# Kernel optimization log

Hardware: AMD Instinct MI355X
Metric: run time of the kernel (lower is better)

The kernel has to match this reference:

```python
import jax, jax.numpy as jnp
import numpy as np

D = 1024      # model dimension
H = 16        # heads
DK = D // H   # head dim
DFF = 4096    # ffn hidden
B, S = 2, 2048
EPS = 1e-6
NEG_SLOPE = 0.01  # torch LeakyReLU default


def setup_inputs() -> dict:
    key = jax.random.key(0)
    ks = jax.random.split(key, 12)
    sd = 1.0 / np.sqrt(D)
    sf = 1.0 / np.sqrt(DFF)
    return {
        "x": jax.random.normal(ks[0], (B, S, D), dtype=jnp.float32),
        "wq": jax.random.uniform(ks[1], (D, D), jnp.float32, -sd, sd),
        "bq": jnp.zeros((D,), jnp.float32),
        "wk": jax.random.uniform(ks[2], (D, D), jnp.float32, -sd, sd),
        "bk": jnp.zeros((D,), jnp.float32),
        "wv": jax.random.uniform(ks[3], (D, D), jnp.float32, -sd, sd),
        "bv": jnp.zeros((D,), jnp.float32),
        "wo": jax.random.uniform(ks[4], (D, D), jnp.float32, -sd, sd),
        "bo": jnp.zeros((D,), jnp.float32),
        "g1": jnp.ones((D,), jnp.float32),
        "b1": jnp.zeros((D,), jnp.float32),
        "w_ff1": jax.random.uniform(ks[5], (D, DFF), jnp.float32, -sd, sd),
        "b_ff1": jnp.zeros((DFF,), jnp.float32),
        "w_ff2": jax.random.uniform(ks[6], (DFF, D), jnp.float32, -sf, sf),
        "b_ff2": jnp.zeros((D,), jnp.float32),
        "g2": jnp.ones((D,), jnp.float32),
        "b2": jnp.zeros((D,), jnp.float32),
    }


def _layernorm(x, g, b):
    mu = jnp.mean(x, axis=-1, keepdims=True)
    var = jnp.mean(jnp.square(x - mu), axis=-1, keepdims=True)
    return (x - mu) * jax.lax.rsqrt(var + EPS) * g + b


def reference(x, wq, bq, wk, bk, wv, bv, wo, bo, g1, b1,
              w_ff1, b_ff1, w_ff2, b_ff2, g2, b2):
    # Multi-head attention
    q = (x @ wq + bq).reshape(B, S, H, DK).transpose(0, 2, 1, 3)  # [B,H,S,DK]
    k = (x @ wk + bk).reshape(B, S, H, DK).transpose(0, 2, 1, 3)
    v = (x @ wv + bv).reshape(B, S, H, DK).transpose(0, 2, 1, 3)
    scores = jnp.einsum('bhqd,bhkd->bhqk', q, k) / np.sqrt(DK)
    attn = jax.nn.softmax(scores, axis=-1)
    ctx = jnp.einsum('bhqk,bhkd->bhqd', attn, v)
    ctx = ctx.transpose(0, 2, 1, 3).reshape(B, S, D)
    attn_out = ctx @ wo + bo
    # residual + LN1 (dropout = identity in eval)
    h = _layernorm(attn_out + x, g1, b1)
    # FFN with LeakyReLU
    ff = jnp.where(h @ w_ff1 + b_ff1 > 0,
                   h @ w_ff1 + b_ff1,
                   NEG_SLOPE * (h @ w_ff1 + b_ff1))
    ff = ff @ w_ff2 + b_ff2
    return _layernorm(ff + h, g2, b2)
```

## Files before the change

### kernel.cpp

```cpp
#include <hip/hip_runtime.h>
#include <math.h>

#define D_MODEL 1024
#define NHEAD   16
#define DKH     64
#define DFF_    4096
#define BB      2
#define SS      2048
#define MTOT    (BB*SS)
#define EPSLN   1e-6f
#define NEG_SLOPE 0.01f

typedef unsigned short u16;
typedef unsigned int   u32;
typedef __bf16 bf16x8 __attribute__((ext_vector_type(8)));
typedef float  f32x4  __attribute__((ext_vector_type(4)));
typedef u16    u16x4  __attribute__((ext_vector_type(4)));

__device__ __forceinline__ u16 f2bf(float f) {
    u32 u = __float_as_uint(f);
    u = (u + 0x7fffu + ((u >> 16) & 1u)) >> 16;
    return (u16)u;
}

__device__ __forceinline__ void gload_lds16(const u16* g, u16* l) {
    __builtin_amdgcn_global_load_lds(
        (const __attribute__((address_space(1))) u32*)g,
        (__attribute__((address_space(3))) u32*)l,
        16, 0, 0);
}

__global__ __launch_bounds__(256)
void f32_to_bf16(const float* __restrict__ in, u16* __restrict__ out) {
    int i = blockIdx.x * 256 + threadIdx.x;
    float4 v = ((const float4*)in)[i];
    u16x4 o = { f2bf(v.x), f2bf(v.y), f2bf(v.z), f2bf(v.w) };
    ((u16x4*)out)[i] = o;
}

__global__ __launch_bounds__(256)
void transpose_w_bf16(const float* __restrict__ W, u16* __restrict__ WT,
                      int K, int N, int out_stride, int out_row_off, float scale)
{
    __shared__ u16 T[64 * 72];
    const int t  = threadIdx.x;
    const int n0 = blockIdx.x * 64;
    const int k0 = blockIdx.y * 64;
    #pragma unroll
    for (int i = 0; i < 4; ++i) {
        int r = i * 16 + (t >> 4);
        int c = (t & 15) * 4;
        float4 v = *(const float4*)&W[(size_t)(k0 + r) * N + n0 + c];
        T[(c + 0) * 72 + r] = f2bf(v.x * scale);
        T[(c + 1) * 72 + r] = f2bf(v.y * scale);
        T[(c + 2) * 72 + r] = f2bf(v.z * scale);
        T[(c + 3) * 72 + r] = f2bf(v.w * scale);
    }
    __syncthreads();
    #pragma unroll
    for (int i = 0; i < 4; ++i) {
        int nr = i * 16 + (t >> 4);
        int kc = (t & 15) * 4;
        u16x4 o = { T[nr*72 + kc], T[nr*72 + kc + 1], T[nr*72 + kc + 2], T[nr*72 + kc + 3] };
        *(u16x4*)&WT[(size_t)(out_row_off + n0 + nr) * out_stride + k0 + kc] = o;
    }
}

__global__ __launch_bounds__(256)
void transpose_v(const u16* __restrict__ QKV, u16* __restrict__ Vt)
{
    __shared__ u16 T[64 * 72];
    const int t  = threadIdx.x;
    const int s0 = blockIdx.x * 64;
    const int bh = blockIdx.y;
    const int b  = bh >> 4, h = bh & 15;
    #pragma unroll
    for (int i = 0; i < 2; ++i) {
        int r = i * 32 + (t >> 3);
        int c = (t & 7) * 8;
        bf16x8 v = *(const bf16x8*)(QKV + ((size_t)b * SS + s0 + r) * 3072 + 2048 + h * 64 + c);
        #pragma unroll
        for (int j = 0; j < 8; ++j) T[(c + j) * 72 + r] = ((const u16*)&v)[j];
    }
    __syncthreads();
    #pragma unroll
    for (int i = 0; i < 2; ++i) {
        int d  = i * 32 + (t >> 3);
        int kc = (t & 7) * 8;
        *(bf16x8*)(Vt + ((size_t)bh * 64 + d) * SS + s0 + kc) = *(const bf16x8*)&T[d * 72 + kc];
    }
}

__global__ __launch_bounds__(256)
void concat_bias(const float* __restrict__ a, const float* __restrict__ b,
                 const float* __restrict__ c, float* __restrict__ out, float qscale) {
    int i = blockIdx.x * 256 + threadIdx.x;
    out[i] = (i < 1024) ? a[i] * qscale : ((i < 2048) ? b[i - 1024] : c[i - 2048]);
}

template<int EPI>
__global__ __launch_bounds__(256)
void gemm_bf16(const u16* __restrict__ A, const u16* __restrict__ BT,
               const float* __restrict__ bias, void* __restrict__ Cout,
               int M, int N, int k_len, int kstride)
{
    __shared__ u16 As[128 * 32];
    __shared__ u16 Bs[128 * 32];
    const int tid  = threadIdx.x;
    const int w    = tid >> 6;
    const int lane = tid & 63;
    const int lm   = lane & 15;
    const int lq   = lane >> 4;
    const int row0 = blockIdx.y * 128;
    const int col0 = blockIdx.x * 128;
    const int k_off = blockIdx.z * k_len;
    const int wrow = (w >> 1) * 64;
    const int wcol = (w & 1) * 64;

    f32x4 acc[4][4] = {};

    const int r_l  = lane >> 2;
    const int q_sw = (lane & 3) ^ ((lane >> 3) & 3);
    const u16* a_src = A  + (size_t)(row0 + w * 32 + r_l) * kstride + k_off + q_sw * 8;
    const u16* b_src = BT + (size_t)(col0 + w * 32 + r_l) * kstride + k_off + q_sw * 8;
    u16* a_dst = &As[(w * 32) * 32];
    u16* b_dst = &Bs[(w * 32) * 32];
    const size_t stepA = (size_t)16 * kstride;

    const int pos = lq ^ ((lm >> 1) & 3);
    const u16* a_rd = &As[(wrow + lm) * 32 + pos * 8];
    const u16* b_rd = &Bs[(wcol + lm) * 32 + pos * 8];

    for (int k0 = 0; k0 < k_len; k0 += 32) {
        gload_lds16(a_src + k0,         a_dst);
        gload_lds16(a_src + k0 + stepA, a_dst + 16 * 32);
        gload_lds16(b_src + k0,         b_dst);
        gload_lds16(b_src + k0 + stepA, b_dst + 16 * 32);
        __syncthreads();
        bf16x8 av[4], bv[4];
        #pragma unroll
        for (int m = 0; m < 4; ++m) av[m] = *(const bf16x8*)(a_rd + m * 16 * 32);
        #pragma unroll
        for (int n = 0; n < 4; ++n) bv[n] = *(const bf16x8*)(b_rd + n * 16 * 32);
        #pragma unroll
        for (int m = 0; m < 4; ++m)
            #pragma unroll
            for (int n = 0; n < 4; ++n)
                acc[m][n] = __builtin_amdgcn_mfma_f32_16x16x32_bf16(av[m], bv[n], acc[m][n], 0, 0, 0);
        __syncthreads();
    }

    float bz[4] = {0.f, 0.f, 0.f, 0.f};
    if (EPI != 3) {
        #pragma unroll
        for (int n = 0; n < 4; ++n) bz[n] = bias[col0 + wcol + n * 16 + lm];
    }
    float* Cz = (float*)Cout + (size_t)blockIdx.z * M * N;

    #pragma unroll
    for (int m = 0; m < 4; ++m) {
        #pragma unroll
        for (int e = 0; e < 4; ++e) {
            int row = row0 + wrow + m * 16 + lq * 4 + e;
            #pragma unroll
            for (int n = 0; n < 4; ++n) {
                int col = col0 + wcol + n * 16 + lm;
                float v = acc[m][n][e] + bz[n];
                if (EPI == 1) v = v > 0.f ? v : NEG_SLOPE * v;
                if (EPI == 3) Cz[(size_t)row * N + col] = v;
                else          ((u16*)Cout)[(size_t)row * N + col] = f2bf(v);
            }
        }
    }
}

__global__ __launch_bounds__(256)
void attn_mfma(const u16* __restrict__ QKV, const u16* __restrict__ Vt,
               u16* __restrict__ ctx)
{
    __shared__ u16 Qs[64 * 72];
    __shared__ u16 Ks[64 * 72];
    __shared__ u16 Vs[64 * 72];
    __shared__ u16 Ps[64 * 72];
    const int tid = threadIdx.x, w = tid >> 6, lane = tid & 63;
    const int lm = lane & 15, lq = lane >> 4;
    const int q0 = blockIdx.x * 64;
    const int bh = blockIdx.y;
    const int b  = bh >> 4, h = bh & 15;
    const size_t row_b = (size_t)b * SS;
    const int ccol = h * DKH;

    const int sr = tid >> 3;
    const int sc = (tid & 7) * 8;

    #pragma unroll
    for (int i = 0; i < 2; ++i) {
        int r = i * 32 + sr;
        *(bf16x8*)&Qs[r * 72 + sc] =
            *(const bf16x8*)(QKV + (row_b + q0 + r) * 3072 + ccol + sc);
    }
    bf16x8 kr[2], vr[2];
    #pragma unroll
    for (int i = 0; i < 2; ++i) {
        int r = i * 32 + sr;
        kr[i] = *(const bf16x8*)(QKV + (row_b + r) * 3072 + 1024 + ccol + sc);
        vr[i] = *(const bf16x8*)(Vt + ((size_t)bh * 64 + r) * SS + sc);
    }
    __syncthreads();
    bf16x8 aq0 = *(const bf16x8*)&Qs[(w * 16 + lm) * 72 + lq * 8];
    bf16x8 aq1 = *(const bf16x8*)&Qs[(w * 16 + lm) * 72 + 32 + lq * 8];

    bf16x8 ones;
    #pragma unroll
    for (int j = 0; j < 8; ++j) ones[j] = (__bf16)1.0f;

    f32x4 o[4] = {};
    f32x4 lacc = {};

    for (int kt = 0; kt < SS / 64; ++kt) {
        __syncthreads();
        #pragma unroll
        for (int i = 0; i < 2; ++i) {
            int r = i * 32 + sr;
            *(bf16x8*)&Ks[r * 72 + sc] = kr[i];
            *(bf16x8*)&Vs[r * 72 + sc] = vr[i];
        }
        const int kn = ((kt + 1) & 31) * 64;
        #pragma unroll
        for (int i = 0; i < 2; ++i) {
            int r = i * 32 + sr;
            kr[i] = *(const bf16x8*)(QKV + (row_b + kn + r) * 3072 + 1024 + ccol + sc);
            vr[i] = *(const bf16x8*)(Vt + ((size_t)bh * 64 + r) * SS + kn + sc);
        }
        __syncthreads();

        f32x4 s[4] = {};
        #pragma unroll
        for (int n = 0; n < 4; ++n) {
            bf16x8 bk0 = *(const bf16x8*)&Ks[(n * 16 + lm) * 72 + lq * 8];
            bf16x8 bk1 = *(const bf16x8*)&Ks[(n * 16 + lm) * 72 + 32 + lq * 8];
            s[n] = __builtin_amdgcn_mfma_f32_16x16x32_bf16(aq0, bk0, s[n], 0, 0, 0);
            s[n] = __builtin_amdgcn_mfma_f32_16x16x32_bf16(aq1, bk1, s[n], 0, 0, 0);
        }
        const int prow = (w * 16 + lq * 4) * 72 + lm;
        #pragma unroll
        for (int n = 0; n < 4; ++n)
            #pragma unroll
            for (int e = 0; e < 4; ++e)
                Ps[prow + e * 72 + n * 16] = f2bf(__builtin_exp2f(s[n][e]));
        __syncthreads();

        bf16x8 ap0 = *(const bf16x8*)&Ps[(w * 16 + lm) * 72 + lq * 8];
        bf16x8 ap1 = *(const bf16x8*)&Ps[(w * 16 + lm) * 72 + 32 + lq * 8];
        #pragma unroll
        for (int n = 0; n < 4; ++n) {
            bf16x8 bv0 = *(const bf16x8*)&Vs[(n * 16 + lm) * 72 + lq * 8];
            bf16x8 bv1 = *(const bf16x8*)&Vs[(n * 16 + lm) * 72 + 32 + lq * 8];
            o[n] = __builtin_amdgcn_mfma_f32_16x16x32_bf16(ap0, bv0, o[n], 0, 0, 0);
            o[n] = __builtin_amdgcn_mfma_f32_16x16x32_bf16(ap1, bv1, o[n], 0, 0, 0);
        }
        lacc = __builtin_amdgcn_mfma_f32_16x16x32_bf16(ap0, ones, lacc, 0, 0, 0);
        lacc = __builtin_amdgcn_mfma_f32_16x16x32_bf16(ap1, ones, lacc, 0, 0, 0);
    }

    #pragma unroll
    for (int e = 0; e < 4; ++e) {
        float inv = 1.0f / lacc[e];
        int row = q0 + w * 16 + lq * 4 + e;
        u16* dst = ctx + (row_b + row) * D_MODEL + ccol;
        #pragma unroll
        for (int n = 0; n < 4; ++n)
            dst[n * 16 + lm] = f2bf(o[n][e] * inv);
    }
}

template<int DUAL>
__global__ __launch_bounds__(256)
void add_ln(const float* __restrict__ C0, const float* __restrict__ C1,
            const float* __restrict__ cbias, const float* __restrict__ resid,
            const float* __restrict__ g, const float* __restrict__ beta,
            float* __restrict__ out, u16* __restrict__ out_bf)
{
    __shared__ float red[8];
    const int row = blockIdx.x;
    const int tid = threadIdx.x;
    float4 v0 = ((const float4*)(C0 + (size_t)row * D_MODEL))[tid];
    float4 v1 = ((const float4*)(C1 + (size_t)row * D_MODEL))[tid];
    float4 cb = ((const float4*)cbias)[tid];
    float4 vr = ((const float4*)(resid + (size_t)row * D_MODEL))[tid];
    float4 v  = { v0.x + v1.x + cb.x + vr.x, v0.y + v1.y + cb.y + vr.y,
                  v0.z + v1.z + cb.z + vr.z, v0.w + v1.w + cb.w + vr.w };
    float s  = v.x + v.y + v.z + v.w;
    float sq = v.x*v.x + v.y*v.y + v.z*v.z + v.w*v.w;
    #pragma unroll
    for (int off = 32; off > 0; off >>= 1) {
        s  += __shfl_down(s,  off, 64);
        sq += __shfl_down(sq, off, 64);
    }
    const int wv = tid >> 6;
    if ((tid & 63) == 0) { red[wv] = s; red[4 + wv] = sq; }
    __syncthreads();
    float st  = red[0] + red[1] + red[2] + red[3];
    float sqt = red[4] + red[5] + red[6] + red[7];
    float mu   = st * (1.0f / D_MODEL);
    float var  = sqt * (1.0f / D_MODEL) - mu * mu;
    float rstd = rsqrtf(var + EPSLN);
    float4 gv = ((const float4*)g)[tid];
    float4 bt = ((const float4*)beta)[tid];
    float4 ov;
    ov.x = (v.x - mu) * rstd * gv.x + bt.x;
    ov.y = (v.y - mu) * rstd * gv.y + bt.y;
    ov.z = (v.z - mu) * rstd * gv.z + bt.z;
    ov.w = (v.w - mu) * rstd * gv.w + bt.w;
    ((float4*)(out + (size_t)row * D_MODEL))[tid] = ov;
    if (DUAL) {
        u16x4 ob = { f2bf(ov.x), f2bf(ov.y), f2bf(ov.z), f2bf(ov.w) };
        ((u16x4*)(out_bf + (size_t)row * D_MODEL))[tid] = ob;
    }
}

extern "C" void kernel_launch(void* const* d_in, const int* in_sizes, int n_in,
                              void* d_out, int out_size, void* d_ws, size_t ws_size,
                              hipStream_t stream) {
    const float* x     = (const float*)d_in[0];
    const float* wq    = (const float*)d_in[1];
    const float* bq    = (const float*)d_in[2];
    const float* wk    = (const float*)d_in[3];
    const float* bk    = (const float*)d_in[4];
    const float* wv    = (const float*)d_in[5];
    const float* bv    = (const float*)d_in[6];
    const float* wo    = (const float*)d_in[7];
    const float* bo    = (const float*)d_in[8];
    const float* g1    = (const float*)d_in[9];
    const float* b1    = (const float*)d_in[10];
    const float* w_ff1 = (const float*)d_in[11];
    const float* b_ff1 = (const float*)d_in[12];
    const float* w_ff2 = (const float*)d_in[13];
    const float* b_ff2 = (const float*)d_in[14];
    const float* g2    = (const float*)d_in[15];
    const float* b2    = (const float*)d_in[16];
    float* out = (float*)d_out;

    const float qscale = 0.18033688011112042f;

    char* W = (char*)d_ws;
    u16*   x_bf    = (u16*)(W + 0);
    u16*   wqkvT   = (u16*)(W + 8388608);
    u16*   woT     = (u16*)(W + 14680064);
    u16*   wff1T   = (u16*)(W + 16777216);
    u16*   wff2T   = (u16*)(W + 25165824);
    u16*   QKV     = (u16*)(W + 33554432);
    u16*   VtG     = (u16*)(W + 58720256);
    float* C0      = (float*)(W + 67108864);
    float* C1      = (float*)(W + 83886080);
    float* h_f     = (float*)(W + 100663296);
    u16*   h_bf    = (u16*)(W + 117440512);
    float* qkv_bias= (float*)(W + 125829120);
    u16*   ctx     = x_bf;
    u16*   ff1_bf  = QKV;

    dim3 blk(256);
    f32_to_bf16<<<4096, blk, 0, stream>>>(x, x_bf);
    transpose_w_bf16<<<dim3(16, 16), blk, 0, stream>>>(wq, wqkvT, 1024, 1024, 1024, 0, qscale);
    transpose_w_bf16<<<dim3(16, 16), blk, 0, stream>>>(wk, wqkvT, 1024, 1024, 1024, 1024, 1.0f);
    transpose_w_bf16<<<dim3(16, 16), blk, 0, stream>>>(wv, wqkvT, 1024, 1024, 1024, 2048, 1.0f);
    transpose_w_bf16<<<dim3(16, 16), blk, 0, stream>>>(wo, woT, 1024, 1024, 1024, 0, 1.0f);
    transpose_w_bf16<<<dim3(64, 16), blk, 0, stream>>>(w_ff1, wff1T, 1024, 4096, 1024, 0, 1.0f);
    transpose_w_bf16<<<dim3(16, 64), blk, 0, stream>>>(w_ff2, wff2T, 4096, 1024, 4096, 0, 1.0f);
    concat_bias<<<12, blk, 0, stream>>>(bq, bk, bv, qkv_bias, qscale);

    gemm_bf16<0><<<dim3(24, 32, 1), blk, 0, stream>>>(x_bf, wqkvT, qkv_bias, QKV, MTOT, 3072, 1024, 1024);
    transpose_v<<<dim3(32, 32), blk, 0, stream>>>(QKV, VtG);
    attn_mfma<<<dim3(32, 32), blk, 0, stream>>>(QKV, VtG, ctx);
    gemm_bf16<3><<<dim3(8, 32, 2), blk, 0, stream>>>(ctx, woT, nullptr, C0, MTOT, 1024, 512, 1024);
    add_ln<1><<<MTOT, blk, 0, stream>>>(C0, C1, bo, x, g1, b1, h_f, h_bf);
    gemm_bf16<1><<<dim3(32, 32, 1), blk, 0, stream>>>(h_bf, wff1T, b_ff1, ff1_bf, MTOT, DFF_, 1024, 1024);
    gemm_bf16<3><<<dim3(8, 32, 2), blk, 0, stream>>>(ff1_bf, wff2T, nullptr, C0, MTOT, 1024, 2048, 4096);
    add_ln<0><<<MTOT, blk, 0, stream>>>(C0, C1, b_ff2, h_f, g2, b2, out, nullptr);
}
```

Baseline: 417.4 us.

## Merge prep kernels, fuse V transpose into QKV GEMM, use bf16 split-K partials

Folds the x conversion, all weight transposes and the bias concat into a single prep launch. The QKV GEMM epilogue now writes V straight into the transposed layout, which removes the transpose_v kernel. Split-K partials and the LN1 residual are stored as bf16 instead of fp32, cutting epilogue and add_ln memory traffic. Attention rounding is simplified to a cheaper round-half-up. These changes lower launch count and bandwidth, but add bf16 rounding error to the partial sums and residual path.

```diff
diff --git a/kernel.cpp b/kernel.cpp
--- a/kernel.cpp
+++ b/kernel.cpp
@@ -22,6 +22,9 @@
     u = (u + 0x7fffu + ((u >> 16) & 1u)) >> 16;
     return (u16)u;
 }
+__device__ __forceinline__ float bf2f(u16 u) {
+    return __uint_as_float(((u32)u) << 16);
+}
 
 __device__ __forceinline__ void gload_lds16(const u16* g, u16* l) {
     __builtin_amdgcn_global_load_lds(
@@ -30,22 +33,13 @@
         16, 0, 0);
 }
 
-__global__ __launch_bounds__(256)
-void f32_to_bf16(const float* __restrict__ in, u16* __restrict__ out) {
-    int i = blockIdx.x * 256 + threadIdx.x;
-    float4 v = ((const float4*)in)[i];
-    u16x4 o = { f2bf(v.x), f2bf(v.y), f2bf(v.z), f2bf(v.w) };
-    ((u16x4*)out)[i] = o;
-}
-
-__global__ __launch_bounds__(256)
-void transpose_w_bf16(const float* __restrict__ W, u16* __restrict__ WT,
-                      int K, int N, int out_stride, int out_row_off, float scale)
+__device__ __forceinline__ void transpose_tile(const float* __restrict__ W,
+        u16* __restrict__ WT, int N, int out_stride, int out_row_off,
+        float scale, int bx, int by, u16* T)
 {
-    __shared__ u16 T[64 * 72];
     const int t  = threadIdx.x;
-    const int n0 = blockIdx.x * 64;
-    const int k0 = blockIdx.y * 64;
+    const int n0 = bx * 64;
+    const int k0 = by * 64;
     #pragma unroll
     for (int i = 0; i < 4; ++i) {
         int r = i * 16 + (t >> 4);
@@ -67,42 +61,56 @@
 }
 
 __global__ __launch_bounds__(256)
-void transpose_v(const u16* __restrict__ QKV, u16* __restrict__ Vt)
+void prep(const float* __restrict__ x, u16* __restrict__ x_bf,
+          const float* __restrict__ wq, const float* __restrict__ wk,
+          const float* __restrict__ wv, const float* __restrict__ wo,
+          const float* __restrict__ wff1, const float* __restrict__ wff2,
+          u16* __restrict__ wqkvT, u16* __restrict__ woT,
+          u16* __restrict__ wff1T, u16* __restrict__ wff2T,
+          const float* __restrict__ bq, const float* __restrict__ bk,
+          const float* __restrict__ bv, float* __restrict__ qkv_bias,
+          float qscale)
 {
     __shared__ u16 T[64 * 72];
-    const int t  = threadIdx.x;
-    const int s0 = blockIdx.x * 64;
-    const int bh = blockIdx.y;
-    const int b  = bh >> 4, h = bh & 15;
-    #pragma unroll
-    for (int i = 0; i < 2; ++i) {
-        int r = i * 32 + (t >> 3);
-        int c = (t & 7) * 8;
-        bf16x8 v = *(const bf16x8*)(QKV + ((size_t)b * SS + s0 + r) * 3072 + 2048 + h * 64 + c);
-        #pragma unroll
-        for (int j = 0; j < 8; ++j) T[(c + j) * 72 + r] = ((const u16*)&v)[j];
-    }
-    __syncthreads();
-    #pragma unroll
-    for (int i = 0; i < 2; ++i) {
-        int d  = i * 32 + (t >> 3);
-        int kc = (t & 7) * 8;
-        *(bf16x8*)(Vt + ((size_t)bh * 64 + d) * SS + s0 + kc) = *(const bf16x8*)&T[d * 72 + kc];
-    }
-}
-
-__global__ __launch_bounds__(256)
-void concat_bias(const float* __restrict__ a, const float* __restrict__ b,
-                 const float* __restrict__ c, float* __restrict__ out, float qscale) {
-    int i = blockIdx.x * 256 + threadIdx.x;
-    out[i] = (i < 1024) ? a[i] * qscale : ((i < 2048) ? b[i - 1024] : c[i - 2048]);
+    int blk = blockIdx.x;
+    if (blk < 4096) {
+        int i = blk * 256 + threadIdx.x;
+        float4 v = ((const float4*)x)[i];
+        u16x4 o = { f2bf(v.x), f2bf(v.y), f2bf(v.z), f2bf(v.w) };
+        ((u16x4*)x_bf)[i] = o;
+        return;
+    }
+    blk -= 4096;
+    if (blk < 1024) {
+        int which = blk >> 8, r = blk & 255;
+        const float* Ws = which == 0 ? wq : which == 1 ? wk : which == 2 ? wv : wo;
+        u16* Wd   = which == 3 ? woT : wqkvT;
+        int off   = which == 3 ? 0 : which * 1024;
+        float sc  = which == 0 ? qscale : 1.0f;
+        transpose_tile(Ws, Wd, 1024, 1024, off, sc, r & 15, r >> 4, T);
+        return;
+    }
+    blk -= 1024;
+    if (blk < 1024) {
+        transpose_tile(wff1, wff1T, 4096, 1024, 0, 1.0f, blk & 63, blk >> 6, T);
+        return;
+    }
+    blk -= 1024;
+    if (blk < 1024) {
+        transpose_tile(wff2, wff2T, 1024, 4096, 0, 1.0f, blk & 15, blk >> 4, T);
+        return;
+    }
+    blk -= 1024;
+    int i = blk * 256 + threadIdx.x;
+    qkv_bias[i] = (i < 1024) ? bq[i] * qscale
+                : (i < 2048) ? bk[i - 1024] : bv[i - 2048];
 }
 
 template<int EPI>
 __global__ __launch_bounds__(256)
 void gemm_bf16(const u16* __restrict__ A, const u16* __restrict__ BT,
                const float* __restrict__ bias, void* __restrict__ Cout,
-               int M, int N, int k_len, int kstride)
+               u16* __restrict__ Vt, int M, int N, int k_len, int kstride)
 {
     __shared__ u16 As[128 * 32];
     __shared__ u16 Bs[128 * 32];
@@ -155,8 +163,24 @@
         #pragma unroll
         for (int n = 0; n < 4; ++n) bz[n] = bias[col0 + wcol + n * 16 + lm];
     }
-    float* Cz = (float*)Cout + (size_t)blockIdx.z * M * N;
-
+
+    if (EPI == 4 && col0 >= 2048) {
+        #pragma unroll
+        for (int m = 0; m < 4; ++m) {
+            int rbase = row0 + wrow + m * 16 + lq * 4;
+            int b = rbase >> 11, s = rbase & 2047;
+            #pragma unroll
+            for (int n = 0; n < 4; ++n) {
+                int c = col0 + wcol + n * 16 + lm - 2048;
+                u16x4 pk = { f2bf(acc[m][n][0] + bz[n]), f2bf(acc[m][n][1] + bz[n]),
+                             f2bf(acc[m][n][2] + bz[n]), f2bf(acc[m][n][3] + bz[n]) };
+                *(u16x4*)&Vt[(size_t)((b * 16 + (c >> 6)) * 64 + (c & 63)) * 2048 + s] = pk;
+            }
+        }
+        return;
+    }
+
+    u16* Cz = (u16*)Cout + (EPI == 3 ? (size_t)blockIdx.z * M * N : 0);
     #pragma unroll
     for (int m = 0; m < 4; ++m) {
         #pragma unroll
@@ -167,8 +191,7 @@
                 int col = col0 + wcol + n * 16 + lm;
                 float v = acc[m][n][e] + bz[n];
                 if (EPI == 1) v = v > 0.f ? v : NEG_SLOPE * v;
-                if (EPI == 3) Cz[(size_t)row * N + col] = v;
-                else          ((u16*)Cout)[(size_t)row * N + col] = f2bf(v);
+                Cz[(size_t)row * N + col] = f2bf(v);
             }
         }
     }
@@ -246,8 +269,11 @@
         #pragma unroll
         for (int n = 0; n < 4; ++n)
             #pragma unroll
-            for (int e = 0; e < 4; ++e)
-                Ps[prow + e * 72 + n * 16] = f2bf(__builtin_exp2f(s[n][e]));
+            for (int e = 0; e < 4; ++e) {
+                float p = __builtin_exp2f(s[n][e]);
+                Ps[prow + e * 72 + n * 16] =
+                    (u16)((__float_as_uint(p) + 0x8000u) >> 16);
+            }
         __syncthreads();
 
         bf16x8 ap0 = *(const bf16x8*)&Ps[(w * 16 + lm) * 72 + lq * 8];
@@ -274,22 +300,30 @@
     }
 }
 
-template<int DUAL>
+template<int OUTF32, int RESBF>
 __global__ __launch_bounds__(256)
-void add_ln(const float* __restrict__ C0, const float* __restrict__ C1,
-            const float* __restrict__ cbias, const float* __restrict__ resid,
+void add_ln(const u16* __restrict__ C0, const u16* __restrict__ C1,
+            const float* __restrict__ cbias, const void* __restrict__ resid,
             const float* __restrict__ g, const float* __restrict__ beta,
-            float* __restrict__ out, u16* __restrict__ out_bf)
+            float* __restrict__ outf, u16* __restrict__ outb)
 {
     __shared__ float red[8];
     const int row = blockIdx.x;
     const int tid = threadIdx.x;
-    float4 v0 = ((const float4*)(C0 + (size_t)row * D_MODEL))[tid];
-    float4 v1 = ((const float4*)(C1 + (size_t)row * D_MODEL))[tid];
+    u16x4 p0 = ((const u16x4*)(C0 + (size_t)row * D_MODEL))[tid];
+    u16x4 p1 = ((const u16x4*)(C1 + (size_t)row * D_MODEL))[tid];
     float4 cb = ((const float4*)cbias)[tid];
-    float4 vr = ((const float4*)(resid + (size_t)row * D_MODEL))[tid];
-    float4 v  = { v0.x + v1.x + cb.x + vr.x, v0.y + v1.y + cb.y + vr.y,
-                  v0.z + v1.z + cb.z + vr.z, v0.w + v1.w + cb.w + vr.w };
+    float4 rr;
+    if (RESBF) {
+        u16x4 rb = ((const u16x4*)((const u16*)resid + (size_t)row * D_MODEL))[tid];
+        rr = { bf2f(rb.x), bf2f(rb.y), bf2f(rb.z), bf2f(rb.w) };
+    } else {
+        rr = ((const float4*)((const float*)resid + (size_t)row * D_MODEL))[tid];
+    }
+    float4 v = { bf2f(p0.x) + bf2f(p1.x) + cb.x + rr.x,
+                 bf2f(p0.y) + bf2f(p1.y) + cb.y + rr.y,
+                 bf2f(p0.z) + bf2f(p1.z) + cb.z + rr.z,
+                 bf2f(p0.w) + bf2f(p1.w) + cb.w + rr.w };
     float s  = v.x + v.y + v.z + v.w;
     float sq = v.x*v.x + v.y*v.y + v.z*v.z + v.w*v.w;
     #pragma unroll
@@ -312,10 +346,11 @@
     ov.y = (v.y - mu) * rstd * gv.y + bt.y;
     ov.z = (v.z - mu) * rstd * gv.z + bt.z;
     ov.w = (v.w - mu) * rstd * gv.w + bt.w;
-    ((float4*)(out + (size_t)row * D_MODEL))[tid] = ov;
-    if (DUAL) {
+    if (OUTF32) {
+        ((float4*)(outf + (size_t)row * D_MODEL))[tid] = ov;
+    } else {
         u16x4 ob = { f2bf(ov.x), f2bf(ov.y), f2bf(ov.z), f2bf(ov.w) };
-        ((u16x4*)(out_bf + (size_t)row * D_MODEL))[tid] = ob;
+        ((u16x4*)(outb + (size_t)row * D_MODEL))[tid] = ob;
     }
 }
 
@@ -351,30 +386,22 @@
     u16*   wff2T   = (u16*)(W + 25165824);
     u16*   QKV     = (u16*)(W + 33554432);
     u16*   VtG     = (u16*)(W + 58720256);
-    float* C0      = (float*)(W + 67108864);
-    float* C1      = (float*)(W + 83886080);
-    float* h_f     = (float*)(W + 100663296);
-    u16*   h_bf    = (u16*)(W + 117440512);
-    float* qkv_bias= (float*)(W + 125829120);
+    u16*   C0      = (u16*)(W + 67108864);
+    u16*   C1      = (u16*)(W + 75497472);
+    u16*   h_bf    = (u16*)(W + 83886080);
+    float* qkv_bias= (float*)(W + 92274688);
     u16*   ctx     = x_bf;
     u16*   ff1_bf  = QKV;
 
     dim3 blk(256);
-    f32_to_bf16<<<4096, blk, 0, stream>>>(x, x_bf);
-    transpose_w_bf16<<<dim3(16, 16), blk, 0, stream>>>(wq, wqkvT, 1024, 1024, 1024, 0, qscale);
-    transpose_w_bf16<<<dim3(16, 16), blk, 0, stream>>>(wk, wqkvT, 1024, 1024, 1024, 1024, 1.0f);
-    transpose_w_bf16<<<dim3(16, 16), blk, 0, stream>>>(wv, wqkvT, 1024, 1024, 1024, 2048, 1.0f);
-    transpose_w_bf16<<<dim3(16, 16), blk, 0, stream>>>(wo, woT, 1024, 1024, 1024, 0, 1.0f);
-    transpose_w_bf16<<<dim3(64, 16), blk, 0, stream>>>(w_ff1, wff1T, 1024, 4096, 1024, 0, 1.0f);
-    transpose_w_bf16<<<dim3(16, 64), blk, 0, stream>>>(w_ff2, wff2T, 4096, 1024, 4096, 0, 1.0f);
-    concat_bias<<<12, blk, 0, stream>>>(bq, bk, bv, qkv_bias, qscale);
-
-    gemm_bf16<0><<<dim3(24, 32, 1), blk, 0, stream>>>(x_bf, wqkvT, qkv_bias, QKV, MTOT, 3072, 1024, 1024);
-    transpose_v<<<dim3(32, 32), blk, 0, stream>>>(QKV, VtG);
+    prep<<<7180, blk, 0, stream>>>(x, x_bf, wq, wk, wv, wo, w_ff1, w_ff2,
+                                   wqkvT, woT, wff1T, wff2T,
+                                   bq, bk, bv, qkv_bias, qscale);
+    gemm_bf16<4><<<dim3(24, 32, 1), blk, 0, stream>>>(x_bf, wqkvT, qkv_bias, QKV, VtG, MTOT, 3072, 1024, 1024);
     attn_mfma<<<dim3(32, 32), blk, 0, stream>>>(QKV, VtG, ctx);
-    gemm_bf16<3><<<dim3(8, 32, 2), blk, 0, stream>>>(ctx, woT, nullptr, C0, MTOT, 1024, 512, 1024);
-    add_ln<1><<<MTOT, blk, 0, stream>>>(C0, C1, bo, x, g1, b1, h_f, h_bf);
-    gemm_bf16<1><<<dim3(32, 32, 1), blk, 0, stream>>>(h_bf, wff1T, b_ff1, ff1_bf, MTOT, DFF_, 1024, 1024);
-    gemm_bf16<3><<<dim3(8, 32, 2), blk, 0, stream>>>(ff1_bf, wff2T, nullptr, C0, MTOT, 1024, 2048, 4096);
-    add_ln<0><<<MTOT, blk, 0, stream>>>(C0, C1, b_ff2, h_f, g2, b2, out, nullptr);
-}
+    gemm_bf16<3><<<dim3(8, 32, 2), blk, 0, stream>>>(ctx, woT, nullptr, C0, nullptr, MTOT, 1024, 512, 1024);
+    add_ln<0, 0><<<MTOT, blk, 0, stream>>>(C0, C1, bo, x, g1, b1, nullptr, h_bf);
+    gemm_bf16<1><<<dim3(32, 32, 1), blk, 0, stream>>>(h_bf, wff1T, b_ff1, ff1_bf, nullptr, MTOT, DFF_, 1024, 1024);
+    gemm_bf16<3><<<dim3(8, 32, 2), blk, 0, stream>>>(ff1_bf, wff2T, nullptr, C0, nullptr, MTOT, 1024, 2048, 4096);
+    add_ln<1, 1><<<MTOT, blk, 0, stream>>>(C0, C1, b_ff2, h_bf, g2, b2, out, nullptr);
+}
```

After: 386.5 us. -7.4%, faster.
